# Kernel tuning notes

Measured on AMD Instinct MI355X. Metric: run time of the kernel, lower is better.

The kernel has to match this reference:

```python
import jax, jax.numpy as jnp
import numpy as np

B, N, FIN, D = 4, 16384, 128, 256
GX, GY = 32, 32
M = GX * GY
NBR = 1
K = (2 * NBR + 1) ** 2
IMG_W, IMG_H = 256.0, 256.0
CELL_W, CELL_H = IMG_W / GX, IMG_H / GY
EPS = 1e-5

# (K,2) offsets, row-major (-n,-n)..(n,n), [dx,dy] like torch _build_offsets_2d
_ys, _xs = np.meshgrid(np.arange(-NBR, NBR + 1), np.arange(-NBR, NBR + 1), indexing='ij')
OFFSETS = jnp.asarray(np.stack([_xs.ravel(), _ys.ravel()], axis=-1), dtype=jnp.int32)  # (K,2)


def setup_inputs() -> dict:
    key = jax.random.key(0)
    ks = jax.random.split(key, 16)
    s = 0.02
    return {
        'features': jax.random.normal(ks[0], (B, N, FIN), dtype=jnp.float32),
        'coords': jax.random.uniform(ks[1], (B, N, 2), dtype=jnp.float32) * IMG_W,
        'valid_mask': jnp.ones((B, N), dtype=bool),
        'Wf': jax.random.normal(ks[2], (FIN, D), dtype=jnp.float32) * s,
        'bf': jnp.zeros((D,), dtype=jnp.float32),
        'Wq': jax.random.normal(ks[3], (D, D), dtype=jnp.float32) * s,
        'bq': jnp.zeros((D,), dtype=jnp.float32),
        'Wk': jax.random.normal(ks[4], (D, D), dtype=jnp.float32) * s,
        'bk': jnp.zeros((D,), dtype=jnp.float32),
        'Wv': jax.random.normal(ks[5], (D, D), dtype=jnp.float32) * s,
        'bv': jnp.zeros((D,), dtype=jnp.float32),
        'Wo': jax.random.normal(ks[6], (D, D), dtype=jnp.float32) * s,
        'bo': jnp.zeros((D,), dtype=jnp.float32),
        'pos_emb': jax.random.normal(ks[7], (K, D), dtype=jnp.float32) * s,
        'gamma': jnp.ones((D,), dtype=jnp.float32),
        'beta': jnp.zeros((D,), dtype=jnp.float32),
    }


def _forward(features, coords, valid_mask, Wf, bf, Wq, bq, Wk, bk, Wv, bv, Wo, bo, pos_emb, gamma, beta):
    feat = features @ Wf + bf  # (B,N,D)

    # coords -> grid cell indices (truncation == torch .long() for nonneg coords)
    ix = jnp.clip((coords[..., 0] / CELL_W).astype(jnp.int32), 0, GX - 1)
    iy = jnp.clip((coords[..., 1] / CELL_H).astype(jnp.int32), 0, GY - 1)
    lin = ix * GY + iy  # (B,N)

    # scatter-mean pool into grid cells
    base = (jnp.arange(B, dtype=jnp.int32) * M)[:, None]
    gid = (lin + base).reshape(-1)  # (B*N,)
    pooled = jax.ops.segment_sum(feat.reshape(-1, D), gid, num_segments=B * M)
    cnt = jax.ops.segment_sum(jnp.ones((B * N,), feat.dtype), gid, num_segments=B * M)
    grid_flat = (pooled / jnp.maximum(cnt, 1.0)[:, None]).reshape(B, M, D)

    # neighbor gather with edge clamping + validity mask
    nbx = ix[:, :, None] + OFFSETS[None, None, :, 0]  # (B,N,K)
    nby = iy[:, :, None] + OFFSETS[None, None, :, 1]
    valid = (nbx >= 0) & (nbx < GX) & (nby >= 0) & (nby < GY)
    lin_n = jnp.clip(nbx, 0, GX - 1) * GY + jnp.clip(nby, 0, GY - 1)  # (B,N,K)
    nbr_feat = jnp.take_along_axis(grid_flat, lin_n.reshape(B, N * K, 1), axis=1).reshape(B, N, K, D)
    nbr_feat = nbr_feat + pos_emb[None, None, :, :]

    # tiny-window attention (1 query vs K neighbors); SDPA scale = 1/sqrt(D)
    Q = feat @ Wq + bq  # (B,N,D)
    Kt = nbr_feat @ Wk + bk  # (B,N,K,D)
    Vt = nbr_feat @ Wv + bv
    scores = jnp.einsum('bnd,bnkd->bnk', Q, Kt) / jnp.sqrt(jnp.float32(D))
    scores = jnp.where(valid, scores, -jnp.inf)
    attn = jax.nn.softmax(scores, axis=-1)
    out = jnp.einsum('bnk,bnkd->bnd', attn, Vt)
    out = out @ Wo + bo

    # residual + layernorm
    h = feat + out
    mu = jnp.mean(h, axis=-1, keepdims=True)
    var = jnp.var(h, axis=-1, keepdims=True)
    h = (h - mu) * jax.lax.rsqrt(var + EPS) * gamma + beta

    return jnp.where(valid_mask[..., None], h, feat)


def reference(features, coords, valid_mask, Wf, bf, Wq, bq, Wk, bk, Wv, bv, Wo, bo, pos_emb, gamma, beta):
    return _forward(features, coords, valid_mask, Wf, bf, Wq, bq, Wk, bk, Wv, bv, Wo, bo, pos_emb, gamma, beta)
```

## Files before the change

kernel.cpp:

```cpp
#include <hip/hip_runtime.h>
#include <math.h>

typedef _Float16 f16;
typedef _Float16 f16x8 __attribute__((ext_vector_type(8)));
typedef float f32x4 __attribute__((ext_vector_type(4)));

constexpr int cB   = 4;
constexpr int cN   = 16384;
constexpr int cFIN = 128;
constexpr int cD   = 256;
constexpr int cGX  = 32;
constexpr int cGY  = 32;
constexpr int cM   = cGX * cGY;
constexpr int cBM  = cB * cM;
constexpr int cBN  = cB * cN;
constexpr int cK   = 9;
constexpr float cEPS = 1e-5f;
constexpr int RPB  = 64;
constexpr int RPG  = 16;
constexpr int GSTR = 264;
constexpr int FSTR = 268;
constexpr int ASTR = 136;

struct f16pair { f16 h; f16 l; };
__device__ inline f16pair split2(float x) {
  f16pair p;
  p.h = (f16)x;
  p.l = (f16)(x - (float)p.h);
  return p;
}

__global__ __launch_bounds__(256)
void k_index(const float* __restrict__ coords, int* __restrict__ lin_arr,
             int* __restrict__ cntI) {
  int p = blockIdx.x * 256 + threadIdx.x;
  if (p >= cBN) return;
  float x = coords[2 * p], y = coords[2 * p + 1];
  int ix = (int)(x * 0.125f);
  int iy = (int)(y * 0.125f);
  ix = min(max(ix, 0), cGX - 1);
  iy = min(max(iy, 0), cGY - 1);
  int lin = ix * cGY + iy;
  lin_arr[p] = lin;
  int b = p / cN;
  atomicAdd(&cntI[b * cM + lin], 1);
}

__global__ __launch_bounds__(1024)
void k_scan(const int* __restrict__ cntI, int* __restrict__ bstart,
            int* __restrict__ bfill) {
  __shared__ int sums[1024];
  int t = threadIdx.x;
  int base = t * 4;
  int v0 = cntI[base], v1 = cntI[base + 1], v2 = cntI[base + 2], v3 = cntI[base + 3];
  sums[t] = v0 + v1 + v2 + v3;
  __syncthreads();
  for (int off = 1; off < 1024; off <<= 1) {
    int val = (t >= off) ? sums[t - off] : 0;
    __syncthreads();
    sums[t] += val;
    __syncthreads();
  }
  int run = (t == 0) ? 0 : sums[t - 1];
  bstart[base] = run;     bfill[base] = run;     run += v0;
  bstart[base + 1] = run; bfill[base + 1] = run; run += v1;
  bstart[base + 2] = run; bfill[base + 2] = run; run += v2;
  bstart[base + 3] = run; bfill[base + 3] = run; run += v3;
  if (t == 1023) bstart[4096] = run;
}

__global__ __launch_bounds__(256)
void k_scatteridx(const int* __restrict__ lin_arr, int* __restrict__ bfill,
                  int* __restrict__ sorted) {
  int p = blockIdx.x * 256 + threadIdx.x;
  if (p >= cBN) return;
  int b = p / cN;
  int gid = b * cM + lin_arr[p];
  int pos = atomicAdd(&bfill[gid], 1);
  sorted[pos] = p;
}

__global__ __launch_bounds__(256)
void k_precompute(const float* __restrict__ Wf, const float* __restrict__ Wq,
                  const float* __restrict__ Wv, const float* __restrict__ Wo,
                  const float* __restrict__ Wk, const float* __restrict__ pe,
                  const float* __restrict__ bf, const float* __restrict__ bq,
                  const float* __restrict__ bv, const float* __restrict__ bo,
                  const float* __restrict__ bk,
                  f16* __restrict__ BTh, f16* __restrict__ BTl,
                  f16* __restrict__ WvoTh, f16* __restrict__ WvoTl,
                  f16* __restrict__ WkTh, f16* __restrict__ WkTl,
                  float* __restrict__ bias2, float* __restrict__ bvo,
                  float* __restrict__ PK, float* __restrict__ PVO) {
  __shared__ float sA[cD];
  __shared__ float sB[cD];
  int bid = blockIdx.x, n = threadIdx.x;
  if (bid < cFIN) {
    int k = bid;
    f16pair pw = split2(Wf[k * cD + n]);
    BTh[n * cFIN + k] = pw.h; BTl[n * cFIN + k] = pw.l;
    float acc = 0.f;
    for (int c = 0; c < cD; c++) acc += Wf[k * cD + c] * Wq[c * cD + n];
    f16pair p = split2(acc);
    BTh[(256 + n) * cFIN + k] = p.h;
    BTl[(256 + n) * cFIN + k] = p.l;
  } else if (bid < cFIN + cD) {
    int k = bid - cFIN;
    float acc = 0.f;
    for (int c = 0; c < cD; c++) acc += Wv[k * cD + c] * Wo[c * cD + n];
    f16pair p = split2(acc);
    WvoTh[n * cD + k] = p.h;
    WvoTl[n * cD + k] = p.l;
  } else if (bid == cFIN + cD) {
    float aq = 0.f, ao = 0.f;
    for (int c = 0; c < cD; c++) {
      aq += bf[c] * Wq[c * cD + n];
      ao += bv[c] * Wo[c * cD + n];
    }
    bias2[n] = bf[n];
    bias2[256 + n] = aq + bq[n];
    bvo[n] = ao + bo[n];
  } else if (bid < cFIN + cD + 1 + cD) {
    int n2 = bid - (cFIN + cD + 1);
    f16pair p = split2(Wk[n * cD + n2]);
    WkTh[n2 * cD + n] = p.h;
    WkTl[n2 * cD + n] = p.l;
  } else {
    int k = bid - (cFIN + cD + 1 + cD);
    sA[n] = pe[k * cD + n];
    __syncthreads();
    float av = 0.f, ak = 0.f;
    for (int c = 0; c < cD; c++) {
      float pv = sA[c];
      av += pv * Wv[c * cD + n];
      ak += pv * Wk[c * cD + n];
    }
    sB[n] = av;
    PK[k * cD + n] = ak + bk[n];
    __syncthreads();
    float ao = 0.f;
    for (int c = 0; c < cD; c++) ao += sB[c] * Wo[c * cD + n];
    PVO[k * cD + n] = ao;
  }
}

__global__ __launch_bounds__(256)
void k_poolsum(const float* __restrict__ features, const int* __restrict__ sorted,
               const int* __restrict__ bstart, f16* __restrict__ Sh,
               f16* __restrict__ Sl, f16* __restrict__ Fh, f16* __restrict__ Fl) {
  __shared__ float Stmp[2][cFIN];
  int gid = blockIdx.x;
  int t = threadIdx.x;
  int half = t >> 7, ch = t & 127;
  int s0 = bstart[gid], s1 = bstart[gid + 1];
  float acc = 0.f;
  for (int i = s0 + half; i < s1; i += 2) {
    int srow = sorted[i];
    float v = features[(size_t)srow * cFIN + ch];
    acc += v;
    f16pair pp = split2(v);
    Fh[(size_t)srow * cFIN + ch] = pp.h;
    Fl[(size_t)srow * cFIN + ch] = pp.l;
  }
  Stmp[half][ch] = acc;
  __syncthreads();
  if (half == 0) {
    f16pair p = split2(Stmp[0][ch] + Stmp[1][ch]);
    Sh[(size_t)gid * cFIN + ch] = p.h;
    Sl[(size_t)gid * cFIN + ch] = p.l;
  }
}

__global__ __launch_bounds__(256)
void k_gemm_gkv(const f16* __restrict__ Sh, const f16* __restrict__ Sl,
                const f16* __restrict__ WfTh, const f16* __restrict__ WfTl,
                const float* __restrict__ bfp, const int* __restrict__ bstart,
                const f16* __restrict__ WkTh, const f16* __restrict__ WkTl,
                const f16* __restrict__ WvoTh, const f16* __restrict__ WvoTl,
                float* __restrict__ GK, float* __restrict__ GVO) {
  __shared__ f16 gshH[RPG * GSTR];
  __shared__ f16 gshL[RPG * GSTR];
  int t = threadIdx.x;
  int w = t >> 6, lane = t & 63;
  int q = lane >> 4, l = lane & 15;
  size_t row0 = (size_t)blockIdx.x * RPG;

  f32x4 acc[4];
#pragma unroll
  for (int tc = 0; tc < 4; tc++) acc[tc] = (f32x4){0.f, 0.f, 0.f, 0.f};

  for (int kk = 0; kk < cFIN; kk += 32) {
    size_t aoff = (row0 + l) * cFIN + q * 8 + kk;
    f16x8 a_h = *(const f16x8*)(Sh + aoff);
    f16x8 a_l = *(const f16x8*)(Sl + aoff);
#pragma unroll
    for (int tc = 0; tc < 4; tc++) {
      size_t boff = (size_t)((w * 4 + tc) * 16 + l) * cFIN + q * 8 + kk;
      f16x8 bh = *(const f16x8*)(WfTh + boff);
      f16x8 bl = *(const f16x8*)(WfTl + boff);
      acc[tc] = __builtin_amdgcn_mfma_f32_16x16x32_f16(a_h, bh, acc[tc], 0, 0, 0);
      acc[tc] = __builtin_amdgcn_mfma_f32_16x16x32_f16(a_h, bl, acc[tc], 0, 0, 0);
      acc[tc] = __builtin_amdgcn_mfma_f32_16x16x32_f16(a_l, bh, acc[tc], 0, 0, 0);
    }
  }
#pragma unroll
  for (int tc = 0; tc < 4; tc++) {
    int col = (w * 4 + tc) * 16 + l;
    float bias = bfp[col];
#pragma unroll
    for (int r = 0; r < 4; r++) {
      size_t row = row0 + q * 4 + r;
      int lr = q * 4 + r;
      int cnt = bstart[row + 1] - bstart[row];
      float g = (cnt > 0) ? (acc[tc][r] / (float)cnt + bias) : 0.f;
      f16pair p = split2(g);
      gshH[lr * GSTR + col] = p.h;
      gshL[lr * GSTR + col] = p.l;
    }
  }
  __syncthreads();

  for (int sel = 0; sel < 2; sel++) {
    const f16* BTh = sel ? WvoTh : WkTh;
    const f16* BTl = sel ? WvoTl : WkTl;
    float* outp = sel ? GVO : GK;
#pragma unroll
    for (int tc = 0; tc < 4; tc++) acc[tc] = (f32x4){0.f, 0.f, 0.f, 0.f};
    for (int kk = 0; kk < cD; kk += 32) {
      int aoff = l * GSTR + q * 8 + kk;
      f16x8 a_h = *(const f16x8*)(gshH + aoff);
      f16x8 a_l = *(const f16x8*)(gshL + aoff);
#pragma unroll
      for (int tc = 0; tc < 4; tc++) {
        size_t boff = (size_t)((w * 4 + tc) * 16 + l) * cD + q * 8 + kk;
        f16x8 bh = *(const f16x8*)(BTh + boff);
        f16x8 bl = *(const f16x8*)(BTl + boff);
        acc[tc] = __builtin_amdgcn_mfma_f32_16x16x32_f16(a_h, bh, acc[tc], 0, 0, 0);
        acc[tc] = __builtin_amdgcn_mfma_f32_16x16x32_f16(a_h, bl, acc[tc], 0, 0, 0);
        acc[tc] = __builtin_amdgcn_mfma_f32_16x16x32_f16(a_l, bh, acc[tc], 0, 0, 0);
      }
    }
#pragma unroll
    for (int tc = 0; tc < 4; tc++) {
      int col = (w * 4 + tc) * 16 + l;
#pragma unroll
      for (int r = 0; r < 4; r++) {
        size_t row = row0 + q * 4 + r;
        outp[row * cD + col] = acc[tc][r];
      }
    }
  }
}

__global__ __launch_bounds__(256)
void k_gemmFQ(const f16* __restrict__ Fh, const f16* __restrict__ Fl,
              const f16* __restrict__ BTh, const f16* __restrict__ BTl,
              const float* __restrict__ bias2,
              float* __restrict__ feat_out, float* __restrict__ Qout) {
  constexpr int APLANE = RPB * ASTR;
  constexpr int ABYTES = 2 * APLANE * 2;
  constexpr int CBYTES = 16 * FSTR * 4;
  __shared__ __align__(16) char smem[ABYTES > CBYTES ? ABYTES : CBYTES];
  f16* sA = (f16*)smem;
  float* sC = (float*)smem;

  int y = blockIdx.y;
  int t = threadIdx.x;
  int w = t >> 6, lane = t & 63;
  int q = lane >> 4, l = lane & 15;
  size_t row0 = (size_t)blockIdx.x * RPB;
  float* outp = y ? Qout : feat_out;

#pragma unroll
  for (int pl = 0; pl < 2; pl++) {
    const f16* S = pl ? Fl : Fh;
    f16* D = sA + pl * APLANE;
#pragma unroll
    for (int k2 = 0; k2 < 4; k2++) {
      int u = k2 * 256 + t;
      int row = u >> 4, chunk = u & 15;
      float4 v = *(const float4*)(S + (row0 + row) * cFIN + chunk * 8);
      *(float4*)(D + row * ASTR + chunk * 8) = v;
    }
  }
  __syncthreads();

  f32x4 acc[4][4];
#pragma unroll
  for (int rs = 0; rs < 4; rs++)
#pragma unroll
    for (int tc = 0; tc < 4; tc++) acc[rs][tc] = (f32x4){0.f, 0.f, 0.f, 0.f};

#pragma unroll
  for (int step = 0; step < 4; step++) {
    const int kk = step * 32;
    f16x8 a_h[4], a_l[4];
#pragma unroll
    for (int rs = 0; rs < 4; rs++) {
      int aoff = (rs * 16 + l) * ASTR + q * 8 + kk;
      a_h[rs] = *(const f16x8*)(sA + aoff);
      a_l[rs] = *(const f16x8*)(sA + APLANE + aoff);
    }
#pragma unroll
    for (int tc = 0; tc < 4; tc++) {
      int ct = y * 16 + w * 4 + tc;
      size_t boff = (size_t)(ct * 16 + l) * cFIN + q * 8 + kk;
      f16x8 bh = *(const f16x8*)(BTh + boff);
      f16x8 bl = *(const f16x8*)(BTl + boff);
#pragma unroll
      for (int rs = 0; rs < 4; rs++) {
        acc[rs][tc] = __builtin_amdgcn_mfma_f32_16x16x32_f16(a_h[rs], bh, acc[rs][tc], 0, 0, 0);
        acc[rs][tc] = __builtin_amdgcn_mfma_f32_16x16x32_f16(a_h[rs], bl, acc[rs][tc], 0, 0, 0);
        acc[rs][tc] = __builtin_amdgcn_mfma_f32_16x16x32_f16(a_l[rs], bh, acc[rs][tc], 0, 0, 0);
      }
    }
  }

#pragma unroll
  for (int rs = 0; rs < 4; rs++) {
    __syncthreads();
#pragma unroll
    for (int tc = 0; tc < 4; tc++) {
      int col = (w * 4 + tc) * 16 + l;
      float b = bias2[y * 256 + col];
#pragma unroll
      for (int r = 0; r < 4; r++)
        sC[(q * 4 + r) * FSTR + col] = acc[rs][tc][r] + b;
    }
    __syncthreads();
#pragma unroll
    for (int j = 0; j < 4; j++) {
      int idx = j * 256 + t;
      int lr = idx >> 6;
      int c4 = (idx & 63) * 4;
      *(float4*)&outp[(row0 + rs * 16 + lr) * cD + c4] =
          *(const float4*)&sC[lr * FSTR + c4];
    }
  }
}

__global__ __launch_bounds__(256)
void k_attn(const float* __restrict__ Qbuf, const float* __restrict__ GK,
            const float* __restrict__ GVO, const float* __restrict__ PK,
            const float* __restrict__ PVO, const int* __restrict__ sorted,
            const int* __restrict__ bstart, const float* __restrict__ bvop,
            const float* __restrict__ gammap, const float* __restrict__ betap,
            float* __restrict__ out) {
  __shared__ float KK[cK][cD];
  __shared__ float VV[cK][cD];
  int gid = blockIdx.x;
  int b = gid / cM;
  int lin = gid % cM;
  int ix = lin / cGY, iy = lin % cGY;
  int t = threadIdx.x;

  int vm = 0;
  for (int k = 0; k < cK; k++) {
    int dx = k % 3 - 1, dy = k / 3 - 1;
    int nx = ix + dx, ny = iy + dy;
    bool v = (nx >= 0 && nx < cGX && ny >= 0 && ny < cGY);
    if (v) vm |= (1 << k);
    int cx = min(max(nx, 0), cGX - 1);
    int cy = min(max(ny, 0), cGY - 1);
    size_t nlin = (size_t)(b * cM + cx * cGY + cy);
    KK[k][t] = GK[nlin * cD + t] + PK[k * cD + t];
    VV[k][t] = GVO[nlin * cD + t] + PVO[k * cD + t];
  }
  __syncthreads();

  int s0 = bstart[gid], s1 = bstart[gid + 1];
  int hw = t >> 5;
  int l32 = t & 31;
  int ch8 = l32 * 8;
  float4 c4a = *(const float4*)&bvop[ch8];
  float4 c4b = *(const float4*)&bvop[ch8 + 4];
  float4 g4a = *(const float4*)&gammap[ch8];
  float4 g4b = *(const float4*)&gammap[ch8 + 4];
  float4 be4a = *(const float4*)&betap[ch8];
  float4 be4b = *(const float4*)&betap[ch8 + 4];

  int ip = s0 + hw;
  if (ip >= s1) return;
  int p = sorted[ip];
  size_t off0 = (size_t)p * cD + ch8;
  float4 qa = *(const float4*)&Qbuf[off0];
  float4 qb = *(const float4*)&Qbuf[off0 + 4];
  float4 fa = *(const float4*)&out[off0];
  float4 fb = *(const float4*)&out[off0 + 4];
  while (true) {
    int ipn = ip + 8;
    bool more = ipn < s1;
    int pn = 0; size_t offn = 0;
    float4 qan = {0.f, 0.f, 0.f, 0.f}, qbn = {0.f, 0.f, 0.f, 0.f};
    float4 fan = {0.f, 0.f, 0.f, 0.f}, fbn = {0.f, 0.f, 0.f, 0.f};
    if (more) {
      pn = sorted[ipn];
      offn = (size_t)pn * cD + ch8;
      qan = *(const float4*)&Qbuf[offn];
      qbn = *(const float4*)&Qbuf[offn + 4];
      fan = *(const float4*)&out[offn];
      fbn = *(const float4*)&out[offn + 4];
    }

    float sc[cK];
#pragma unroll
    for (int k = 0; k < cK; k++) {
      float4 k0 = *(const float4*)&KK[k][ch8];
      float4 k1 = *(const float4*)&KK[k][ch8 + 4];
      sc[k] = qa.x * k0.x + qa.y * k0.y + qa.z * k0.z + qa.w * k0.w +
              qb.x * k1.x + qb.y * k1.y + qb.z * k1.z + qb.w * k1.w;
    }
#pragma unroll
    for (int off = 16; off > 0; off >>= 1)
#pragma unroll
      for (int k = 0; k < cK; k++) sc[k] += __shfl_xor(sc[k], off, 32);

    float mx = -1e30f;
#pragma unroll
    for (int k = 0; k < cK; k++)
      if ((vm >> k) & 1) mx = fmaxf(mx, sc[k] * 0.0625f);
    float e[cK], ssum = 0.f;
#pragma unroll
    for (int k = 0; k < cK; k++) {
      float v = ((vm >> k) & 1) ? __expf(sc[k] * 0.0625f - mx) : 0.f;
      e[k] = v; ssum += v;
    }
    float inv = 1.f / ssum;
    float4 oa = {0.f, 0.f, 0.f, 0.f}, ob = {0.f, 0.f, 0.f, 0.f};
#pragma unroll
    for (int k = 0; k < cK; k++) {
      float a = e[k] * inv;
      float4 v0 = *(const float4*)&VV[k][ch8];
      float4 v1 = *(const float4*)&VV[k][ch8 + 4];
      oa.x += a * v0.x; oa.y += a * v0.y; oa.z += a * v0.z; oa.w += a * v0.w;
      ob.x += a * v1.x; ob.y += a * v1.y; ob.z += a * v1.z; ob.w += a * v1.w;
    }
    float4 ha, hb;
    ha.x = fa.x + oa.x + c4a.x; ha.y = fa.y + oa.y + c4a.y;
    ha.z = fa.z + oa.z + c4a.z; ha.w = fa.w + oa.w + c4a.w;
    hb.x = fb.x + ob.x + c4b.x; hb.y = fb.y + ob.y + c4b.y;
    hb.z = fb.z + ob.z + c4b.z; hb.w = fb.w + ob.w + c4b.w;
    float s = ha.x + ha.y + ha.z + ha.w + hb.x + hb.y + hb.z + hb.w;
    float ss = ha.x * ha.x + ha.y * ha.y + ha.z * ha.z + ha.w * ha.w +
               hb.x * hb.x + hb.y * hb.y + hb.z * hb.z + hb.w * hb.w;
#pragma unroll
    for (int o2 = 16; o2 > 0; o2 >>= 1) {
      s += __shfl_xor(s, o2, 32);
      ss += __shfl_xor(ss, o2, 32);
    }
    float mu = s * (1.f / cD);
    float var = ss * (1.f / cD) - mu * mu;
    float rsr = rsqrtf(var + cEPS);
    float4 ra, rb;
    ra.x = (ha.x - mu) * rsr * g4a.x + be4a.x;
    ra.y = (ha.y - mu) * rsr * g4a.y + be4a.y;
    ra.z = (ha.z - mu) * rsr * g4a.z + be4a.z;
    ra.w = (ha.w - mu) * rsr * g4a.w + be4a.w;
    rb.x = (hb.x - mu) * rsr * g4b.x + be4b.x;
    rb.y = (hb.y - mu) * rsr * g4b.y + be4b.y;
    rb.z = (hb.z - mu) * rsr * g4b.z + be4b.z;
    rb.w = (hb.w - mu) * rsr * g4b.w + be4b.w;
    *(float4*)&out[off0] = ra;
    *(float4*)&out[off0 + 4] = rb;

    if (!more) break;
    ip = ipn; p = pn; off0 = offn;
    qa = qan; qb = qbn; fa = fan; fb = fbn;
  }
}

extern "C" void kernel_launch(void* const* d_in, const int* in_sizes, int n_in,
                              void* d_out, int out_size, void* d_ws, size_t ws_size,
                              hipStream_t stream) {
  (void)in_sizes; (void)n_in; (void)out_size; (void)ws_size;
  const float* features = (const float*)d_in[0];
  const float* coords   = (const float*)d_in[1];
  const float* Wf = (const float*)d_in[3];
  const float* bf = (const float*)d_in[4];
  const float* Wq = (const float*)d_in[5];
  const float* bq = (const float*)d_in[6];
  const float* Wk = (const float*)d_in[7];
  const float* bk = (const float*)d_in[8];
  const float* Wv = (const float*)d_in[9];
  const float* bv = (const float*)d_in[10];
  const float* Wo = (const float*)d_in[11];
  const float* bo = (const float*)d_in[12];
  const float* pe = (const float*)d_in[13];
  const float* gm = (const float*)d_in[14];
  const float* bt = (const float*)d_in[15];
  float* out = (float*)d_out;

  char* ws = (char*)d_ws;
  size_t o = 0;
  auto take = [&](size_t bytes) -> void* {
    void* p = ws + o;
    o = (o + bytes + 255) & ~(size_t)255;
    return p;
  };
  int* lin_arr = (int*)take((size_t)cBN * 4);
  int* sorted  = (int*)take((size_t)cBN * 4);
  int* bstart  = (int*)take((size_t)(cBM + 1) * 4);
  int* bfill   = (int*)take((size_t)cBM * 4);
  int* cntI    = (int*)take((size_t)cBM * 4);
  float* GK    = (float*)take((size_t)cBM * cD * 4);
  float* GVO   = (float*)take((size_t)cBM * cD * 4);
  float* PK    = (float*)take((size_t)cK * cD * 4);
  float* PVO   = (float*)take((size_t)cK * cD * 4);
  float* Qbuf  = (float*)take((size_t)cBN * cD * 4);
  f16* Fh      = (f16*)take((size_t)cBN * cFIN * 2);
  f16* Fl      = (f16*)take((size_t)cBN * cFIN * 2);
  f16* BTh     = (f16*)take((size_t)512 * cFIN * 2);
  f16* BTl     = (f16*)take((size_t)512 * cFIN * 2);
  f16* WvoTh   = (f16*)take((size_t)cD * cD * 2);
  f16* WvoTl   = (f16*)take((size_t)cD * cD * 2);
  f16* WkTh    = (f16*)take((size_t)cD * cD * 2);
  f16* WkTl    = (f16*)take((size_t)cD * cD * 2);
  f16* Sh      = (f16*)take((size_t)cBM * cFIN * 2);
  f16* Sl      = (f16*)take((size_t)cBM * cFIN * 2);
  float* bias2 = (float*)take((size_t)512 * 4);
  float* bvo   = (float*)take((size_t)cD * 4);

  (void)hipMemsetAsync(cntI, 0, (size_t)cBM * 4, stream);

  k_index<<<cBN / 256, 256, 0, stream>>>(coords, lin_arr, cntI);
  k_scan<<<1, 1024, 0, stream>>>(cntI, bstart, bfill);
  k_scatteridx<<<cBN / 256, 256, 0, stream>>>(lin_arr, bfill, sorted);
  k_precompute<<<cFIN + cD + 1 + cD + cK, 256, 0, stream>>>(
      Wf, Wq, Wv, Wo, Wk, pe, bf, bq, bv, bo, bk,
      BTh, BTl, WvoTh, WvoTl, WkTh, WkTl, bias2, bvo, PK, PVO);
  k_poolsum<<<cBM, 256, 0, stream>>>(features, sorted, bstart, Sh, Sl, Fh, Fl);
  k_gemm_gkv<<<cBM / RPG, 256, 0, stream>>>(Sh, Sl, BTh, BTl, bf, bstart,
                                            WkTh, WkTl, WvoTh, WvoTl, GK, GVO);
  dim3 gFQ(cBN / RPB, 2);
  k_gemmFQ<<<gFQ, 256, 0, stream>>>(Fh, Fl, BTh, BTl, bias2, out, Qbuf);
  k_attn<<<cBM, 256, 0, stream>>>(Qbuf, GK, GVO, PK, PVO, sorted, bstart,
                                  bvo, gm, bt, out);
}
```

Before: 305.1 us.

## Merge gemmFQ y-blocks into 512-thread blocks and widen attention blocks

k_gemmFQ now runs one 512-thread block per 64-row tile. The two halves (feat and Q outputs) share a single staged A tile in shared memory instead of two blocks each loading it. k_attn also moves to 512 threads: the neighbor K/V staging is split across two thread halves, and 16 half-warps process points with a strided channel layout (ca, ca+128). The explicit software prefetch of the next point's Q and feat is dropped. Larger blocks may reduce occupancy, and losing the prefetch may expose load latency.

Result: slower. 327.4 us (+7.3%).

```diff
diff --git a/kernel.cpp b/kernel.cpp
--- a/kernel.cpp
+++ b/kernel.cpp
@@ -252,36 +252,32 @@
   }
 }
 
-__global__ __launch_bounds__(256)
+__global__ __launch_bounds__(512)
 void k_gemmFQ(const f16* __restrict__ Fh, const f16* __restrict__ Fl,
               const f16* __restrict__ BTh, const f16* __restrict__ BTl,
               const float* __restrict__ bias2,
               float* __restrict__ feat_out, float* __restrict__ Qout) {
   constexpr int APLANE = RPB * ASTR;
   constexpr int ABYTES = 2 * APLANE * 2;
-  constexpr int CBYTES = 16 * FSTR * 4;
-  __shared__ __align__(16) char smem[ABYTES > CBYTES ? ABYTES : CBYTES];
+  __shared__ __align__(16) char smem[ABYTES];
   f16* sA = (f16*)smem;
   float* sC = (float*)smem;
 
-  int y = blockIdx.y;
   int t = threadIdx.x;
-  int w = t >> 6, lane = t & 63;
+  int w = t >> 6;
+  int y = w >> 2;
+  int wl = w & 3;
+  int lane = t & 63;
   int q = lane >> 4, l = lane & 15;
   size_t row0 = (size_t)blockIdx.x * RPB;
-  float* outp = y ? Qout : feat_out;
-
-#pragma unroll
-  for (int pl = 0; pl < 2; pl++) {
+
+#pragma unroll
+  for (int k2 = 0; k2 < 4; k2++) {
+    int u = k2 * 512 + t;
+    int pl = u >> 10, row = (u >> 4) & 63, chunk = u & 15;
     const f16* S = pl ? Fl : Fh;
-    f16* D = sA + pl * APLANE;
-#pragma unroll
-    for (int k2 = 0; k2 < 4; k2++) {
-      int u = k2 * 256 + t;
-      int row = u >> 4, chunk = u & 15;
-      float4 v = *(const float4*)(S + (row0 + row) * cFIN + chunk * 8);
-      *(float4*)(D + row * ASTR + chunk * 8) = v;
-    }
+    float4 v = *(const float4*)(S + (row0 + row) * cFIN + chunk * 8);
+    *(float4*)(sA + pl * APLANE + row * ASTR + chunk * 8) = v;
   }
   __syncthreads();
 
@@ -303,7 +299,7 @@
     }
 #pragma unroll
     for (int tc = 0; tc < 4; tc++) {
-      int ct = y * 16 + w * 4 + tc;
+      int ct = y * 16 + wl * 4 + tc;
       size_t boff = (size_t)(ct * 16 + l) * cFIN + q * 8 + kk;
       f16x8 bh = *(const f16x8*)(BTh + boff);
       f16x8 bl = *(const f16x8*)(BTl + boff);
@@ -319,27 +315,31 @@
 #pragma unroll
   for (int rs = 0; rs < 4; rs++) {
     __syncthreads();
+    float* myC = sC + y * 16 * FSTR;
 #pragma unroll
     for (int tc = 0; tc < 4; tc++) {
-      int col = (w * 4 + tc) * 16 + l;
+      int col = (wl * 4 + tc) * 16 + l;
       float b = bias2[y * 256 + col];
 #pragma unroll
       for (int r = 0; r < 4; r++)
-        sC[(q * 4 + r) * FSTR + col] = acc[rs][tc][r] + b;
+        myC[(q * 4 + r) * FSTR + col] = acc[rs][tc][r] + b;
     }
     __syncthreads();
 #pragma unroll
     for (int j = 0; j < 4; j++) {
-      int idx = j * 256 + t;
-      int lr = idx >> 6;
-      int c4 = (idx & 63) * 4;
-      *(float4*)&outp[(row0 + rs * 16 + lr) * cD + c4] =
-          *(const float4*)&sC[lr * FSTR + c4];
-    }
-  }
-}
-
-__global__ __launch_bounds__(256)
+      int idx = j * 512 + t;
+      int buf = idx >> 10;
+      int within = idx & 1023;
+      int lr = within >> 6;
+      int c4 = (within & 63) * 4;
+      float* dst = buf ? Qout : feat_out;
+      *(float4*)&dst[(row0 + rs * 16 + lr) * cD + c4] =
+          *(const float4*)&sC[buf * 16 * FSTR + lr * FSTR + c4];
+    }
+  }
+}
+
+__global__ __launch_bounds__(512)
 void k_attn(const float* __restrict__ Qbuf, const float* __restrict__ GK,
             const float* __restrict__ GVO, const float* __restrict__ PK,
             const float* __restrict__ PVO, const int* __restrict__ sorted,
@@ -355,58 +355,49 @@
   int t = threadIdx.x;
 
   int vm = 0;
+#pragma unroll
   for (int k = 0; k < cK; k++) {
     int dx = k % 3 - 1, dy = k / 3 - 1;
     int nx = ix + dx, ny = iy + dy;
-    bool v = (nx >= 0 && nx < cGX && ny >= 0 && ny < cGY);
-    if (v) vm |= (1 << k);
-    int cx = min(max(nx, 0), cGX - 1);
-    int cy = min(max(ny, 0), cGY - 1);
-    size_t nlin = (size_t)(b * cM + cx * cGY + cy);
-    KK[k][t] = GK[nlin * cD + t] + PK[k * cD + t];
-    VV[k][t] = GVO[nlin * cD + t] + PVO[k * cD + t];
+    if (nx >= 0 && nx < cGX && ny >= 0 && ny < cGY) vm |= (1 << k);
+  }
+  {
+    int half = t >> 8, ch = t & 255;
+    for (int k = half; k < cK; k += 2) {
+      int dx = k % 3 - 1, dy = k / 3 - 1;
+      int cx = min(max(ix + dx, 0), cGX - 1);
+      int cy = min(max(iy + dy, 0), cGY - 1);
+      size_t nlin = (size_t)(b * cM + cx * cGY + cy);
+      KK[k][ch] = GK[nlin * cD + ch] + PK[k * cD + ch];
+      VV[k][ch] = GVO[nlin * cD + ch] + PVO[k * cD + ch];
+    }
   }
   __syncthreads();
 
   int s0 = bstart[gid], s1 = bstart[gid + 1];
   int hw = t >> 5;
   int l32 = t & 31;
-  int ch8 = l32 * 8;
-  float4 c4a = *(const float4*)&bvop[ch8];
-  float4 c4b = *(const float4*)&bvop[ch8 + 4];
-  float4 g4a = *(const float4*)&gammap[ch8];
-  float4 g4b = *(const float4*)&gammap[ch8 + 4];
-  float4 be4a = *(const float4*)&betap[ch8];
-  float4 be4b = *(const float4*)&betap[ch8 + 4];
-
-  int ip = s0 + hw;
-  if (ip >= s1) return;
-  int p = sorted[ip];
-  size_t off0 = (size_t)p * cD + ch8;
-  float4 qa = *(const float4*)&Qbuf[off0];
-  float4 qb = *(const float4*)&Qbuf[off0 + 4];
-  float4 fa = *(const float4*)&out[off0];
-  float4 fb = *(const float4*)&out[off0 + 4];
-  while (true) {
-    int ipn = ip + 8;
-    bool more = ipn < s1;
-    int pn = 0; size_t offn = 0;
-    float4 qan = {0.f, 0.f, 0.f, 0.f}, qbn = {0.f, 0.f, 0.f, 0.f};
-    float4 fan = {0.f, 0.f, 0.f, 0.f}, fbn = {0.f, 0.f, 0.f, 0.f};
-    if (more) {
-      pn = sorted[ipn];
-      offn = (size_t)pn * cD + ch8;
-      qan = *(const float4*)&Qbuf[offn];
-      qbn = *(const float4*)&Qbuf[offn + 4];
-      fan = *(const float4*)&out[offn];
-      fbn = *(const float4*)&out[offn + 4];
-    }
+  int ca = l32 * 4, cb = ca + 128;
+  float4 c4a = *(const float4*)&bvop[ca];
+  float4 c4b = *(const float4*)&bvop[cb];
+  float4 g4a = *(const float4*)&gammap[ca];
+  float4 g4b = *(const float4*)&gammap[cb];
+  float4 be4a = *(const float4*)&betap[ca];
+  float4 be4b = *(const float4*)&betap[cb];
+
+  for (int ip = s0 + hw; ip < s1; ip += 16) {
+    int p = sorted[ip];
+    size_t off0 = (size_t)p * cD;
+    float4 qa = *(const float4*)&Qbuf[off0 + ca];
+    float4 qb = *(const float4*)&Qbuf[off0 + cb];
+    float4 fa = *(const float4*)&out[off0 + ca];
+    float4 fb = *(const float4*)&out[off0 + cb];
 
     float sc[cK];
 #pragma unroll
     for (int k = 0; k < cK; k++) {
-      float4 k0 = *(const float4*)&KK[k][ch8];
-      float4 k1 = *(const float4*)&KK[k][ch8 + 4];
+      float4 k0 = *(const float4*)&KK[k][ca];
+      float4 k1 = *(const float4*)&KK[k][cb];
       sc[k] = qa.x * k0.x + qa.y * k0.y + qa.z * k0.z + qa.w * k0.w +
               qb.x * k1.x + qb.y * k1.y + qb.z * k1.z + qb.w * k1.w;
     }
@@ -430,8 +421,8 @@
 #pragma unroll
     for (int k = 0; k < cK; k++) {
       float a = e[k] * inv;
-      float4 v0 = *(const float4*)&VV[k][ch8];
-      float4 v1 = *(const float4*)&VV[k][ch8 + 4];
+      float4 v0 = *(const float4*)&VV[k][ca];
+      float4 v1 = *(const float4*)&VV[k][cb];
       oa.x += a * v0.x; oa.y += a * v0.y; oa.z += a * v0.z; oa.w += a * v0.w;
       ob.x += a * v1.x; ob.y += a * v1.y; ob.z += a * v1.z; ob.w += a * v1.w;
     }
@@ -460,12 +451,8 @@
     rb.y = (hb.y - mu) * rsr * g4b.y + be4b.y;
     rb.z = (hb.z - mu) * rsr * g4b.z + be4b.z;
     rb.w = (hb.w - mu) * rsr * g4b.w + be4b.w;
-    *(float4*)&out[off0] = ra;
-    *(float4*)&out[off0 + 4] = rb;
-
-    if (!more) break;
-    ip = ipn; p = pn; off0 = offn;
-    qa = qan; qb = qbn; fa = fan; fb = fbn;
+    *(float4*)&out[off0 + ca] = ra;
+    *(float4*)&out[off0 + cb] = rb;
   }
 }
 
@@ -531,8 +518,7 @@
   k_poolsum<<<cBM, 256, 0, stream>>>(features, sorted, bstart, Sh, Sl, Fh, Fl);
   k_gemm_gkv<<<cBM / RPG, 256, 0, stream>>>(Sh, Sl, BTh, BTl, bf, bstart,
                                             WkTh, WkTl, WvoTh, WvoTl, GK, GVO);
-  dim3 gFQ(cBN / RPB, 2);
-  k_gemmFQ<<<gFQ, 256, 0, stream>>>(Fh, Fl, BTh, BTl, bias2, out, Qbuf);
-  k_attn<<<cBM, 256, 0, stream>>>(Qbuf, GK, GVO, PK, PVO, sorted, bstart,
+  k_gemmFQ<<<cBN / RPB, 512, 0, stream>>>(Fh, Fl, BTh, BTl, bias2, out, Qbuf);
+  k_attn<<<cBM, 512, 0, stream>>>(Qbuf, GK, GVO, PK, PVO, sorted, bstart,
                                   bvo, gm, bt, out);
 }
```
